# Performance work log

Measured on AMD Instinct MI355X. Metric: run time of the kernel, lower is better.

The kernel has to match this reference:

```python
import jax, jax.numpy as jnp
import numpy as np

WIN = 9  # win_size from init

def setup_inputs() -> dict:
    key = jax.random.key(0)
    ks = jax.random.split(key, 4)
    N, L, C, U = 8, 4096, 256, 256
    x = jax.random.normal(ks[0], (N, L, C), dtype=jnp.float32)
    W_qry = jax.random.normal(ks[1], (C, U), dtype=jnp.float32) * 0.05
    W_key = jax.random.normal(ks[2], (C, U), dtype=jnp.float32) * 0.05
    v = jax.random.normal(ks[3], (U,), dtype=jnp.float32) * 0.05
    b = jnp.zeros((U,), dtype=jnp.float32)
    return {"x": x, "W_qry": W_qry, "W_key": W_key, "v": v, "b": b}

def reference(x, W_qry, W_key, v, b):
    N, L, C = x.shape
    n_w = L - WIN + 1
    # sliding-window gather: idx[w, s] = w + s
    idx = jnp.arange(n_w)[:, None] + jnp.arange(WIN)[None, :]
    x_win = x[:, idx]
    x_ctr = x[:, WIN // 2 : WIN // 2 + n_w]                    # [N, n_w, C]
    key = jnp.einsum('nwsc,cu->nwsu', x_win, W_key)
    qry = jnp.einsum('nwc,cu->nwu', x_ctr, W_qry)              # [N, n_w, U]
    score = jnp.einsum('nwsu,u->nws', jnp.tanh(qry[:, :, None, :] + key + b), v)
    weight = jax.nn.softmax(score, axis=2)                     # softmax over window dim
    out = jnp.einsum('nwsc,nws->nwc', x_win, weight)           # [N, n_w, C]
    return out
```

## Files before the change

### kernel.cpp

```cpp
#include <hip/hip_runtime.h>
#include <hip/hip_bf16.h>

#define WIN   9
#define NB    8
#define LL    4096
#define CC    256
#define UU    256
#define NW    (LL - WIN + 1)
#define MROWS (NB * LL)

typedef unsigned short ushort;
typedef __attribute__((ext_vector_type(8))) unsigned short ushort8v;
typedef __attribute__((ext_vector_type(4))) unsigned short ushort4v;
typedef __attribute__((ext_vector_type(8))) short short8v;
typedef __attribute__((ext_vector_type(4))) float f32x4;

__device__ __forceinline__ float bf16_to_f(ushort u) {
    return __uint_as_float(((unsigned int)u) << 16);
}
__device__ __forceinline__ ushort f2bf(float f) {
    __hip_bfloat16 h = __float2bfloat16(f);
    return *reinterpret_cast<ushort*>(&h);
}
__device__ __forceinline__ float fast_tanh(float x) {
    float e = __expf(2.0f * x);
    return 1.0f - 2.0f * __builtin_amdgcn_rcpf(e + 1.0f);
}

__global__ __launch_bounds__(256) void cvt_x(const float* __restrict__ X,
                                             ushort* __restrict__ Xb) {
    size_t i = ((size_t)blockIdx.x * 256 + threadIdx.x) * 8;
    float4 v0 = *reinterpret_cast<const float4*>(X + i);
    float4 v1 = *reinterpret_cast<const float4*>(X + i + 4);
    ushort8v o;
    o[0] = f2bf(v0.x); o[1] = f2bf(v0.y); o[2] = f2bf(v0.z); o[3] = f2bf(v0.w);
    o[4] = f2bf(v1.x); o[5] = f2bf(v1.y); o[6] = f2bf(v1.z); o[7] = f2bf(v1.w);
    *reinterpret_cast<ushort8v*>(Xb + i) = o;
}

__global__ __launch_bounds__(256) void transpose_w(const float* __restrict__ Wk,
                                                   const float* __restrict__ Wq,
                                                   ushort* __restrict__ WkT,
                                                   ushort* __restrict__ WqT) {
    const float* W = blockIdx.z ? Wq : Wk;
    ushort* O = blockIdx.z ? WqT : WkT;
    __shared__ float t[32][33];
    int c0 = blockIdx.x * 32, u0 = blockIdx.y * 32;
    int tr = threadIdx.x >> 3, tc = (threadIdx.x & 7) * 4;
    float4 v = *reinterpret_cast<const float4*>(&W[(size_t)(c0 + tr) * UU + u0 + tc]);
    t[tr][tc + 0] = v.x; t[tr][tc + 1] = v.y; t[tr][tc + 2] = v.z; t[tr][tc + 3] = v.w;
    __syncthreads();
    ushort4v o;
    #pragma unroll
    for (int i = 0; i < 4; ++i) o[i] = f2bf(t[tc + i][tr]);
    *reinterpret_cast<ushort4v*>(&O[(size_t)(u0 + tr) * CC + c0 + tc]) = o;
}

__global__ __launch_bounds__(256) void gemm_mfma(const ushort* __restrict__ Xb,
                                                 const ushort* __restrict__ WkT,
                                                 const ushort* __restrict__ WqT,
                                                 ushort* __restrict__ Kout,
                                                 ushort* __restrict__ Qout) {
    const int xb = blockIdx.x;
    const ushort* WT = (xb < 4) ? WkT : WqT;
    ushort* Out = (xb < 4) ? Kout : Qout;
    const int nbase = (xb & 3) * 64;
    const int m0 = blockIdx.y * 128;

    __shared__ ushort As[128 * 40];
    __shared__ ushort Bs[64 * 40];

    const int tid = threadIdx.x;
    const int wid = tid >> 6, lane = tid & 63;
    const int wr = wid >> 1, wc = wid & 1;
    const int lrow = lane & 15, lk = (lane >> 4) * 8;

    f32x4 acc[4][2] = {};

    const int srow = tid >> 1, shalf = tid & 1;
    const ushort* aSrc = Xb + (size_t)(m0 + srow) * CC + shalf * 16;
    ushort* aDst = &As[srow * 40 + shalf * 16];
    const int bu = tid >> 2, bk = (tid & 3) * 8;
    const ushort* bSrc = WT + (size_t)(nbase + bu) * CC + bk;
    ushort* bDst = &Bs[bu * 40 + bk];

    for (int k0 = 0; k0 < CC; k0 += 32) {
        ushort8v a0 = *reinterpret_cast<const ushort8v*>(aSrc + k0);
        ushort8v a1 = *reinterpret_cast<const ushort8v*>(aSrc + k0 + 8);
        ushort8v b0 = *reinterpret_cast<const ushort8v*>(bSrc + k0);
        *reinterpret_cast<ushort8v*>(aDst) = a0;
        *reinterpret_cast<ushort8v*>(aDst + 8) = a1;
        *reinterpret_cast<ushort8v*>(bDst) = b0;
        __syncthreads();

        short8v af[4], bf[2];
        #pragma unroll
        for (int m = 0; m < 4; ++m)
            af[m] = *reinterpret_cast<const short8v*>(&As[(wr * 64 + m * 16 + lrow) * 40 + lk]);
        #pragma unroll
        for (int n = 0; n < 2; ++n)
            bf[n] = *reinterpret_cast<const short8v*>(&Bs[(wc * 32 + n * 16 + lrow) * 40 + lk]);
        #pragma unroll
        for (int m = 0; m < 4; ++m)
            #pragma unroll
            for (int n = 0; n < 2; ++n)
                acc[m][n] = __builtin_amdgcn_mfma_f32_16x16x32_bf16(af[m], bf[n], acc[m][n], 0, 0, 0);
        __syncthreads();
    }

    const int orow = m0 + wr * 64 + (lane >> 4) * 4;
    const int ocol = nbase + wc * 32 + lrow;
    #pragma unroll
    for (int m = 0; m < 4; ++m)
        #pragma unroll
        for (int n = 0; n < 2; ++n)
            #pragma unroll
            for (int j = 0; j < 4; ++j)
                Out[(size_t)(orow + m * 16 + j) * UU + ocol + n * 16] = f2bf(acc[m][n][j]);
}

__global__ __launch_bounds__(256) void attn_smooth(
    const float* __restrict__ X,
    const ushort* __restrict__ Kb,
    const ushort* __restrict__ Qb,
    const float* __restrict__ v,
    const float* __restrict__ b,
    float* __restrict__ out) {
    const int wave = threadIdx.x >> 6;
    const int lane = threadIdx.x & 63;
    const int bid = blockIdx.x;
    const int nb = (bid & 7) * 1022 + (bid >> 3);
    const int item = nb * 4 + wave;
    const int n = item / NW;
    const int w = item % NW;
    const int u0 = lane * 4;

    const size_t rowbase = (size_t)(n * LL + w);

    float4 bv = *reinterpret_cast<const float4*>(&b[u0]);
    float4 vv = *reinterpret_cast<const float4*>(&v[u0]);

    ushort4 qu = *reinterpret_cast<const ushort4*>(&Qb[(rowbase + WIN / 2) * UU + u0]);
    float qb0 = bf16_to_f(qu.x) + bv.x;
    float qb1 = bf16_to_f(qu.y) + bv.y;
    float qb2 = bf16_to_f(qu.z) + bv.z;
    float qb3 = bf16_to_f(qu.w) + bv.w;

    float p[WIN];
    #pragma unroll
    for (int s = 0; s < WIN; ++s) {
        ushort4 ku = *reinterpret_cast<const ushort4*>(&Kb[(rowbase + s) * UU + u0]);
        float t;
        t  = vv.x * fast_tanh(qb0 + bf16_to_f(ku.x));
        t += vv.y * fast_tanh(qb1 + bf16_to_f(ku.y));
        t += vv.z * fast_tanh(qb2 + bf16_to_f(ku.z));
        t += vv.w * fast_tanh(qb3 + bf16_to_f(ku.w));
        p[s] = t;
    }
    #pragma unroll
    for (int off = 32; off; off >>= 1)
        #pragma unroll
        for (int s = 0; s < WIN; ++s)
            p[s] += __shfl_xor(p[s], off);

    float m = p[0];
    #pragma unroll
    for (int s = 1; s < WIN; ++s) m = fmaxf(m, p[s]);
    float e[WIN];
    float sum = 0.0f;
    #pragma unroll
    for (int s = 0; s < WIN; ++s) { e[s] = __expf(p[s] - m); sum += e[s]; }
    float inv = 1.0f / sum;

    float4 acc = {0.0f, 0.0f, 0.0f, 0.0f};
    #pragma unroll
    for (int s = 0; s < WIN; ++s) {
        float ws = e[s] * inv;
        float4 xv = *reinterpret_cast<const float4*>(&X[(rowbase + s) * CC + u0]);
        acc.x = fmaf(ws, xv.x, acc.x);
        acc.y = fmaf(ws, xv.y, acc.y);
        acc.z = fmaf(ws, xv.z, acc.z);
        acc.w = fmaf(ws, xv.w, acc.w);
    }
    *reinterpret_cast<float4*>(&out[((size_t)n * NW + w) * CC + u0]) = acc;
}

extern "C" void kernel_launch(void* const* d_in, const int* in_sizes, int n_in,
                              void* d_out, int out_size, void* d_ws, size_t ws_size,
                              hipStream_t stream) {
    const float* x  = (const float*)d_in[0];
    const float* Wq = (const float*)d_in[1];
    const float* Wk = (const float*)d_in[2];
    const float* v  = (const float*)d_in[3];
    const float* b  = (const float*)d_in[4];
    float* out = (float*)d_out;

    const size_t MU = (size_t)MROWS * UU;
    ushort* Kbuf = (ushort*)d_ws;
    ushort* Qbuf = Kbuf + MU;
    ushort* Xb   = Qbuf + MU;
    ushort* WkT  = Xb + MU;
    ushort* WqT  = WkT + (size_t)CC * UU;

    cvt_x<<<MROWS * CC / (256 * 8), 256, 0, stream>>>(x, Xb);
    transpose_w<<<dim3(8, 8, 2), 256, 0, stream>>>(Wk, Wq, WkT, WqT);
    gemm_mfma<<<dim3(8, MROWS / 128), 256, 0, stream>>>(Xb, WkT, WqT, Kbuf, Qbuf);
    attn_smooth<<<(NB * NW) / 4, 256, 0, stream>>>(x, Kbuf, Qbuf, v, b, out);
}
```

Measured before the change: 151.1 us.

## Fuse x bf16 conversion into GEMM and load operands directly from global memory

Removes the separate cvt_x pass. The GEMM now reads fp32 x straight from global memory, converts it to bf16 in registers, and loads weight fragments directly without shared-memory staging or barriers. Each 512-thread block computes all 512 K and Q output columns for 128 rows, so x is read once per row block instead of once per column block. In exchange, each wave holds 32 accumulator tiles, which raises register pressure and may limit occupancy. Operand loads are also strided and uncoalesced and depend on cache hits.

```diff
diff --git a/kernel.cpp b/kernel.cpp
--- a/kernel.cpp
+++ b/kernel.cpp
@@ -27,17 +27,6 @@
     return 1.0f - 2.0f * __builtin_amdgcn_rcpf(e + 1.0f);
 }
 
-__global__ __launch_bounds__(256) void cvt_x(const float* __restrict__ X,
-                                             ushort* __restrict__ Xb) {
-    size_t i = ((size_t)blockIdx.x * 256 + threadIdx.x) * 8;
-    float4 v0 = *reinterpret_cast<const float4*>(X + i);
-    float4 v1 = *reinterpret_cast<const float4*>(X + i + 4);
-    ushort8v o;
-    o[0] = f2bf(v0.x); o[1] = f2bf(v0.y); o[2] = f2bf(v0.z); o[3] = f2bf(v0.w);
-    o[4] = f2bf(v1.x); o[5] = f2bf(v1.y); o[6] = f2bf(v1.z); o[7] = f2bf(v1.w);
-    *reinterpret_cast<ushort8v*>(Xb + i) = o;
-}
-
 __global__ __launch_bounds__(256) void transpose_w(const float* __restrict__ Wk,
                                                    const float* __restrict__ Wq,
                                                    ushort* __restrict__ WkT,
@@ -56,67 +45,58 @@
     *reinterpret_cast<ushort4v*>(&O[(size_t)(u0 + tr) * CC + c0 + tc]) = o;
 }
 
-__global__ __launch_bounds__(256) void gemm_mfma(const ushort* __restrict__ Xb,
-                                                 const ushort* __restrict__ WkT,
-                                                 const ushort* __restrict__ WqT,
-                                                 ushort* __restrict__ Kout,
-                                                 ushort* __restrict__ Qout) {
-    const int xb = blockIdx.x;
-    const ushort* WT = (xb < 4) ? WkT : WqT;
-    ushort* Out = (xb < 4) ? Kout : Qout;
-    const int nbase = (xb & 3) * 64;
-    const int m0 = blockIdx.y * 128;
-
-    __shared__ ushort As[128 * 40];
-    __shared__ ushort Bs[64 * 40];
-
-    const int tid = threadIdx.x;
-    const int wid = tid >> 6, lane = tid & 63;
-    const int wr = wid >> 1, wc = wid & 1;
+__global__ __launch_bounds__(512) void gemm_direct(const float* __restrict__ X,
+                                                   const ushort* __restrict__ WkT,
+                                                   const ushort* __restrict__ WqT,
+                                                   ushort* __restrict__ Kout,
+                                                   ushort* __restrict__ Qout) {
+    const int m0 = blockIdx.x * 128;
+    const int wid = threadIdx.x >> 6, lane = threadIdx.x & 63;
+    const int wr = wid >> 2;
+    const int wc = wid & 3;
     const int lrow = lane & 15, lk = (lane >> 4) * 8;
 
-    f32x4 acc[4][2] = {};
+    const ushort* WT = (wc < 2) ? WkT : WqT;
+    ushort* Out = (wc < 2) ? Kout : Qout;
+    const int nbase = (wc & 1) * 128;
 
-    const int srow = tid >> 1, shalf = tid & 1;
-    const ushort* aSrc = Xb + (size_t)(m0 + srow) * CC + shalf * 16;
-    ushort* aDst = &As[srow * 40 + shalf * 16];
-    const int bu = tid >> 2, bk = (tid & 3) * 8;
-    const ushort* bSrc = WT + (size_t)(nbase + bu) * CC + bk;
-    ushort* bDst = &Bs[bu * 40 + bk];
+    const float*  aBase = X  + (size_t)(m0 + wr * 64 + lrow) * CC + lk;
+    const ushort* bBase = WT + (size_t)(nbase + lrow) * CC + lk;
 
+    f32x4 acc[4][8] = {};
+
+    #pragma unroll 2
     for (int k0 = 0; k0 < CC; k0 += 32) {
-        ushort8v a0 = *reinterpret_cast<const ushort8v*>(aSrc + k0);
-        ushort8v a1 = *reinterpret_cast<const ushort8v*>(aSrc + k0 + 8);
-        ushort8v b0 = *reinterpret_cast<const ushort8v*>(bSrc + k0);
-        *reinterpret_cast<ushort8v*>(aDst) = a0;
-        *reinterpret_cast<ushort8v*>(aDst + 8) = a1;
-        *reinterpret_cast<ushort8v*>(bDst) = b0;
-        __syncthreads();
-
-        short8v af[4], bf[2];
+        short8v af[4], bf[8];
         #pragma unroll
-        for (int m = 0; m < 4; ++m)
-            af[m] = *reinterpret_cast<const short8v*>(&As[(wr * 64 + m * 16 + lrow) * 40 + lk]);
+        for (int m = 0; m < 4; ++m) {
+            const float* p = aBase + (size_t)m * 16 * CC + k0;
+            float4 a0 = *reinterpret_cast<const float4*>(p);
+            float4 a1 = *reinterpret_cast<const float4*>(p + 4);
+            ushort8v t;
+            t[0] = f2bf(a0.x); t[1] = f2bf(a0.y); t[2] = f2bf(a0.z); t[3] = f2bf(a0.w);
+            t[4] = f2bf(a1.x); t[5] = f2bf(a1.y); t[6] = f2bf(a1.z); t[7] = f2bf(a1.w);
+            af[m] = *reinterpret_cast<short8v*>(&t);
+        }
         #pragma unroll
-        for (int n = 0; n < 2; ++n)
-            bf[n] = *reinterpret_cast<const short8v*>(&Bs[(wc * 32 + n * 16 + lrow) * 40 + lk]);
+        for (int n = 0; n < 8; ++n)
+            bf[n] = *reinterpret_cast<const short8v*>(bBase + (size_t)n * 16 * CC + k0);
         #pragma unroll
         for (int m = 0; m < 4; ++m)
             #pragma unroll
-            for (int n = 0; n < 2; ++n)
+            for (int n = 0; n < 8; ++n)
                 acc[m][n] = __builtin_amdgcn_mfma_f32_16x16x32_bf16(af[m], bf[n], acc[m][n], 0, 0, 0);
-        __syncthreads();
     }
 
-    const int orow = m0 + wr * 64 + (lane >> 4) * 4;
-    const int ocol = nbase + wc * 32 + lrow;
+    const int orow0 = m0 + wr * 64 + (lane >> 4) * 4;
+    const int ocol0 = nbase + lrow;
     #pragma unroll
     for (int m = 0; m < 4; ++m)
         #pragma unroll
-        for (int n = 0; n < 2; ++n)
+        for (int n = 0; n < 8; ++n)
             #pragma unroll
             for (int j = 0; j < 4; ++j)
-                Out[(size_t)(orow + m * 16 + j) * UU + ocol + n * 16] = f2bf(acc[m][n][j]);
+                Out[(size_t)(orow0 + m * 16 + j) * UU + ocol0 + n * 16] = f2bf(acc[m][n][j]);
 }
 
 __global__ __launch_bounds__(256) void attn_smooth(
@@ -198,12 +178,10 @@
     const size_t MU = (size_t)MROWS * UU;
     ushort* Kbuf = (ushort*)d_ws;
     ushort* Qbuf = Kbuf + MU;
-    ushort* Xb   = Qbuf + MU;
-    ushort* WkT  = Xb + MU;
+    ushort* WkT  = Qbuf + MU;
     ushort* WqT  = WkT + (size_t)CC * UU;
 
-    cvt_x<<<MROWS * CC / (256 * 8), 256, 0, stream>>>(x, Xb);
     transpose_w<<<dim3(8, 8, 2), 256, 0, stream>>>(Wk, Wq, WkT, WqT);
-    gemm_mfma<<<dim3(8, MROWS / 128), 256, 0, stream>>>(Xb, WkT, WqT, Kbuf, Qbuf);
+    gemm_direct<<<MROWS / 128, 512, 0, stream>>>(x, WkT, WqT, Kbuf, Qbuf);
     attn_smooth<<<(NB * NW) / 4, 256, 0, stream>>>(x, Kbuf, Qbuf, v, b, out);
 }
```

New measurement: 152.7 us. No clear change (+1.1%).

## Rewrite projection GEMM with direct global-to-LDS loads, swizzle, larger tiles; read bf16 x

Applied to the files above, without the earlier changes.

The K/Q projection GEMM now uses 128x128 output tiles with BK=64. Tiles are loaded straight from global memory into LDS with global_load_lds, using an XOR swizzle to avoid bank conflicts. WkT and WqT are treated as one contiguous 512-row weight matrix. The attention kernel reads the bf16 copy of x instead of fp32 x for the weighted sum, which halves that traffic but lowers output precision. This relies on WqT following WkT in the workspace and on the bf16 error in the output staying within tolerance.

```diff
diff --git a/kernel.cpp b/kernel.cpp
--- a/kernel.cpp
+++ b/kernel.cpp
@@ -8,6 +8,9 @@
 #define UU    256
 #define NW    (LL - WIN + 1)
 #define MROWS (NB * LL)
+
+#define BM 128
+#define BK 64
 
 typedef unsigned short ushort;
 typedef __attribute__((ext_vector_type(8))) unsigned short ushort8v;
@@ -56,71 +59,85 @@
     *reinterpret_cast<ushort4v*>(&O[(size_t)(u0 + tr) * CC + c0 + tc]) = o;
 }
 
-__global__ __launch_bounds__(256) void gemm_mfma(const ushort* __restrict__ Xb,
-                                                 const ushort* __restrict__ WkT,
-                                                 const ushort* __restrict__ WqT,
-                                                 ushort* __restrict__ Kout,
-                                                 ushort* __restrict__ Qout) {
-    const int xb = blockIdx.x;
-    const ushort* WT = (xb < 4) ? WkT : WqT;
-    ushort* Out = (xb < 4) ? Kout : Qout;
-    const int nbase = (xb & 3) * 64;
-    const int m0 = blockIdx.y * 128;
-
-    __shared__ ushort As[128 * 40];
-    __shared__ ushort Bs[64 * 40];
+__global__ __launch_bounds__(256, 2) void gemm_lds(const ushort* __restrict__ Xb,
+                                                   const ushort* __restrict__ WTall,
+                                                   ushort* __restrict__ Kout,
+                                                   ushort* __restrict__ Qout) {
+    const int m0 = (blockIdx.x & 255) * BM;
+    const int nt = blockIdx.x >> 8;
+    const int n0 = nt * 128;
+
+    __shared__ ushort As[BM * BK];
+    __shared__ ushort Bs[BM * BK];
 
     const int tid = threadIdx.x;
     const int wid = tid >> 6, lane = tid & 63;
     const int wr = wid >> 1, wc = wid & 1;
-    const int lrow = lane & 15, lk = (lane >> 4) * 8;
-
-    f32x4 acc[4][2] = {};
-
-    const int srow = tid >> 1, shalf = tid & 1;
-    const ushort* aSrc = Xb + (size_t)(m0 + srow) * CC + shalf * 16;
-    ushort* aDst = &As[srow * 40 + shalf * 16];
-    const int bu = tid >> 2, bk = (tid & 3) * 8;
-    const ushort* bSrc = WT + (size_t)(nbase + bu) * CC + bk;
-    ushort* bDst = &Bs[bu * 40 + bk];
-
-    for (int k0 = 0; k0 < CC; k0 += 32) {
-        ushort8v a0 = *reinterpret_cast<const ushort8v*>(aSrc + k0);
-        ushort8v a1 = *reinterpret_cast<const ushort8v*>(aSrc + k0 + 8);
-        ushort8v b0 = *reinterpret_cast<const ushort8v*>(bSrc + k0);
-        *reinterpret_cast<ushort8v*>(aDst) = a0;
-        *reinterpret_cast<ushort8v*>(aDst + 8) = a1;
-        *reinterpret_cast<ushort8v*>(bDst) = b0;
+    const int lrow = lane & 15;
+    const int lkc  = lane >> 4;
+
+    const int srow_in_issue = wid * 8 + (lane >> 3);
+    const int schunk = lane & 7;
+
+    f32x4 acc[4][4] = {};
+
+    for (int k0 = 0; k0 < CC; k0 += BK) {
+        #pragma unroll
+        for (int i = 0; i < 4; ++i) {
+            int row = i * 32 + srow_in_issue;
+            int ca  = schunk ^ (row & 7);
+            const ushort* srcA = Xb    + (size_t)(m0 + row) * CC + k0 + ca * 8;
+            const ushort* srcB = WTall + (size_t)(n0 + row) * CC + k0 + ca * 8;
+            ushort* dstA = As + i * 2048 + wid * 512;
+            ushort* dstB = Bs + i * 2048 + wid * 512;
+            __builtin_amdgcn_global_load_lds(
+                (const __attribute__((address_space(1))) void*)srcA,
+                (__attribute__((address_space(3))) void*)dstA, 16, 0, 0);
+            __builtin_amdgcn_global_load_lds(
+                (const __attribute__((address_space(1))) void*)srcB,
+                (__attribute__((address_space(3))) void*)dstB, 16, 0, 0);
+        }
         __syncthreads();
 
-        short8v af[4], bf[2];
-        #pragma unroll
-        for (int m = 0; m < 4; ++m)
-            af[m] = *reinterpret_cast<const short8v*>(&As[(wr * 64 + m * 16 + lrow) * 40 + lk]);
-        #pragma unroll
-        for (int n = 0; n < 2; ++n)
-            bf[n] = *reinterpret_cast<const short8v*>(&Bs[(wc * 32 + n * 16 + lrow) * 40 + lk]);
-        #pragma unroll
-        for (int m = 0; m < 4; ++m)
-            #pragma unroll
-            for (int n = 0; n < 2; ++n)
-                acc[m][n] = __builtin_amdgcn_mfma_f32_16x16x32_bf16(af[m], bf[n], acc[m][n], 0, 0, 0);
+        #pragma unroll
+        for (int ks = 0; ks < 2; ++ks) {
+            short8v af[4], bq[4];
+            #pragma unroll
+            for (int m = 0; m < 4; ++m) {
+                int r = wr * 64 + m * 16 + lrow;
+                int cc = ks * 4 + lkc;
+                af[m] = *reinterpret_cast<const short8v*>(As + r * 64 + (cc ^ (r & 7)) * 8);
+            }
+            #pragma unroll
+            for (int n = 0; n < 4; ++n) {
+                int r = wc * 64 + n * 16 + lrow;
+                int cc = ks * 4 + lkc;
+                bq[n] = *reinterpret_cast<const short8v*>(Bs + r * 64 + (cc ^ (r & 7)) * 8);
+            }
+            #pragma unroll
+            for (int m = 0; m < 4; ++m)
+                #pragma unroll
+                for (int n = 0; n < 4; ++n)
+                    acc[m][n] = __builtin_amdgcn_mfma_f32_16x16x32_bf16(af[m], bq[n], acc[m][n], 0, 0, 0);
+        }
         __syncthreads();
     }
 
-    const int orow = m0 + wr * 64 + (lane >> 4) * 4;
-    const int ocol = nbase + wc * 32 + lrow;
+    ushort* Out = (nt < 2) ? Kout : Qout;
+    const int colbase = (nt & 1) * 128 + wc * 64;
+    const int rowbase = m0 + wr * 64 + (lane >> 4) * 4;
     #pragma unroll
     for (int m = 0; m < 4; ++m)
         #pragma unroll
-        for (int n = 0; n < 2; ++n)
+        for (int n = 0; n < 4; ++n)
             #pragma unroll
             for (int j = 0; j < 4; ++j)
-                Out[(size_t)(orow + m * 16 + j) * UU + ocol + n * 16] = f2bf(acc[m][n][j]);
+                Out[(size_t)(rowbase + m * 16 + j) * UU + colbase + n * 16 + lrow] =
+                    f2bf(acc[m][n][j]);
 }
 
 __global__ __launch_bounds__(256) void attn_smooth(
-    const float* __restrict__ X,
+    const ushort* __restrict__ Xb,
     const ushort* __restrict__ Kb,
     const ushort* __restrict__ Qb,
     const float* __restrict__ v,
@@ -176,11 +193,11 @@
     #pragma unroll
     for (int s = 0; s < WIN; ++s) {
         float ws = e[s] * inv;
-        float4 xv = *reinterpret_cast<const float4*>(&X[(rowbase + s) * CC + u0]);
-        acc.x = fmaf(ws, xv.x, acc.x);
-        acc.y = fmaf(ws, xv.y, acc.y);
-        acc.z = fmaf(ws, xv.z, acc.z);
-        acc.w = fmaf(ws, xv.w, acc.w);
+        ushort4 xv = *reinterpret_cast<const ushort4*>(&Xb[(rowbase + s) * CC + u0]);
+        acc.x = fmaf(ws, bf16_to_f(xv.x), acc.x);
+        acc.y = fmaf(ws, bf16_to_f(xv.y), acc.y);
+        acc.z = fmaf(ws, bf16_to_f(xv.z), acc.z);
+        acc.w = fmaf(ws, bf16_to_f(xv.w), acc.w);
     }
     *reinterpret_cast<float4*>(&out[((size_t)n * NW + w) * CC + u0]) = acc;
 }
@@ -204,6 +221,6 @@
 
     cvt_x<<<MROWS * CC / (256 * 8), 256, 0, stream>>>(x, Xb);
     transpose_w<<<dim3(8, 8, 2), 256, 0, stream>>>(Wk, Wq, WkT, WqT);
-    gemm_mfma<<<dim3(8, MROWS / 128), 256, 0, stream>>>(Xb, WkT, WqT, Kbuf, Qbuf);
-    attn_smooth<<<(NB * NW) / 4, 256, 0, stream>>>(x, Kbuf, Qbuf, v, b, out);
-}
+    gemm_lds<<<1024, 256, 0, stream>>>(Xb, WkT, Kbuf, Qbuf);
+    attn_smooth<<<(NB * NW) / 4, 256, 0, stream>>>(Xb, Kbuf, Qbuf, v, b, out);
+}
```

Result: faster. 145.7 us (-3.6%).
